# Kernel tuning notes

Measured on AMD Instinct MI355X. Metric: run time of the kernel, lower is better.

Reference implementation:

```python
import jax, jax.numpy as jnp
import numpy as np
from jax import lax


def setup_inputs() -> dict:
    key = jax.random.key(0)
    k1, k2 = jax.random.split(key)
    B, T, D = 32, 4096, 256
    x = jax.random.normal(k1, (B, T, D), dtype=jnp.float32)
    logit_alpha = jax.random.normal(k2, (D,), dtype=jnp.float32)
    return {"x": x, "logit_alpha": logit_alpha}


def _ema_scan(x, alpha):
    # Linear recurrence y_t = a_t * y_{t-1} + b_t is associative; use a
    # log-depth parallel scan over T instead of a sequential loop.
    B, T, D = x.shape
    one_minus_alpha = 1.0 - alpha  # [D]
    # y_0 = x_0  ->  a_0 = 0, b_0 = x_0 ; for t>=1: a_t = alpha, b_t = (1-alpha)*x_t
    a = jnp.concatenate(
        [jnp.zeros((B, 1, D), x.dtype), jnp.broadcast_to(alpha, (B, T - 1, D))],
        axis=1,
    )
    b = jnp.concatenate([x[:, :1, :], one_minus_alpha * x[:, 1:, :]], axis=1)

    def combine(e1, e2):
        a1, b1 = e1
        a2, b2 = e2
        return a1 * a2, a2 * b1 + b2

    _, y = lax.associative_scan(combine, (a, b), axis=1)
    return y


def reference(x, logit_alpha):
    # x: [B, T, D]; per-feature alpha in (0,1)
    alpha = jax.nn.sigmoid(logit_alpha)  # [D]
    return _ema_scan(x, alpha)
```

## Files before the change

kernel.cpp:

```cpp
#include <hip/hip_runtime.h>

#define B_  32
#define T_  4096
#define D_  256
#define D4_ 64

typedef float f32x4 __attribute__((ext_vector_type(4)));

__device__ __forceinline__ f32x4 sigmoid4(f32x4 v) {
    f32x4 r;
    r[0] = 1.0f / (1.0f + expf(-v[0]));
    r[1] = 1.0f / (1.0f + expf(-v[1]));
    r[2] = 1.0f / (1.0f + expf(-v[2]));
    r[3] = 1.0f / (1.0f + expf(-v[3]));
    return r;
}

__global__ __launch_bounds__(256) void ema_carry(
    const f32x4* __restrict__ x, const f32x4* __restrict__ la,
    f32x4* __restrict__ E, int NC, int L) {
    const int wid  = threadIdx.x >> 6;
    const int lane = threadIdx.x & 63;
    const int g = blockIdx.x * 4 + wid;
    const int b = g / NC;
    const int c = g % NC;

    const f32x4 al = sigmoid4(la[lane]);
    const f32x4 om = 1.0f - al;

    size_t idx = ((size_t)b * T_ + (size_t)c * L) * D4_ + lane;
    f32x4 y = 0.0f;
    int i0 = 0;
    if (c == 0) {
        y = x[idx];
        idx += D4_;
        i0 = 1;
    }
    #pragma unroll 8
    for (int i = i0; i < L; ++i) {
        y = al * y + om * x[idx];
        idx += D4_;
    }
    E[(size_t)g * D4_ + lane] = y;
}

__global__ __launch_bounds__(256) void ema_apply(
    const f32x4* __restrict__ x, const f32x4* __restrict__ la,
    const f32x4* __restrict__ E, f32x4* __restrict__ yout,
    int NC, int L, int log2L) {
    const int wid  = threadIdx.x >> 6;
    const int lane = threadIdx.x & 63;
    const int g = blockIdx.x * 4 + wid;
    const int b = g / NC;
    const int c = g % NC;

    const f32x4 al = sigmoid4(la[lane]);
    const f32x4 om = 1.0f - al;

    f32x4 aL = al;
    for (int k = 0; k < log2L; ++k) aL = aL * aL;
    const f32x4 aL2 = aL * aL;
    const f32x4 aL4 = aL2 * aL2;
    const f32x4 aL8 = aL4 * aL4;

    const f32x4* Eb = E + ((size_t)b * NC) * D4_ + lane;
    f32x4 H = 0.0f;
    int j = 0;
    for (; j + 8 <= c; j += 8) {
        f32x4 e0 = Eb[(size_t)(j + 0) * D4_];
        f32x4 e1 = Eb[(size_t)(j + 1) * D4_];
        f32x4 e2 = Eb[(size_t)(j + 2) * D4_];
        f32x4 e3 = Eb[(size_t)(j + 3) * D4_];
        f32x4 e4 = Eb[(size_t)(j + 4) * D4_];
        f32x4 e5 = Eb[(size_t)(j + 5) * D4_];
        f32x4 e6 = Eb[(size_t)(j + 6) * D4_];
        f32x4 e7 = Eb[(size_t)(j + 7) * D4_];
        f32x4 t = e0;
        t = t * aL + e1;
        t = t * aL + e2;
        t = t * aL + e3;
        t = t * aL + e4;
        t = t * aL + e5;
        t = t * aL + e6;
        t = t * aL + e7;
        H = aL8 * H + t;
    }
    for (; j < c; ++j)
        H = aL * H + Eb[(size_t)j * D4_];

    size_t idx = ((size_t)b * T_ + (size_t)c * L) * D4_ + lane;
    f32x4 acc = H;
    int i0 = 0;
    if (c == 0) {
        acc = x[idx];
        __builtin_nontemporal_store(acc, &yout[idx]);
        idx += D4_;
        i0 = 1;
    }
    #pragma unroll 8
    for (int i = i0; i < L; ++i) {
        acc = al * acc + om * x[idx];
        __builtin_nontemporal_store(acc, &yout[idx]);
        idx += D4_;
    }
}

extern "C" void kernel_launch(void* const* d_in, const int* in_sizes, int n_in,
                              void* d_out, int out_size, void* d_ws, size_t ws_size,
                              hipStream_t stream) {
    const f32x4* x  = (const f32x4*)d_in[0];
    const f32x4* la = (const f32x4*)d_in[1];
    f32x4* out = (f32x4*)d_out;

    int NC = 128;
    while (NC > 1 && (size_t)B_ * NC * D_ * sizeof(float) > ws_size) NC >>= 1;
    const int L = T_ / NC;
    int log2L = 0;
    while ((1 << log2L) < L) ++log2L;

    f32x4* E = (f32x4*)d_ws;
    const int ntasks = B_ * NC;
    dim3 blk(256);
    dim3 grd(ntasks / 4);

    ema_carry<<<grd, blk, 0, stream>>>(x, la, E, NC, L);
    ema_apply<<<grd, blk, 0, stream>>>(x, la, E, out, NC, L, log2L);
}
```

Measured before the change: 74.80 us.

## Restructure EMA as local scan plus carry fixup pass over output

Replaces the carry-then-recompute scheme with a first pass that writes the locally scanned output and chunk carries, and a second pass that adds the propagated carry times powers of alpha to the stored output. This removes the second read of x and the recurrence recompute in the apply pass, but adds a read-modify-write of the output. The chunk count is halved, which reduces carry work but also the number of parallel waves.

```diff
diff --git a/kernel.cpp b/kernel.cpp
--- a/kernel.cpp
+++ b/kernel.cpp
@@ -16,9 +16,9 @@
     return r;
 }
 
-__global__ __launch_bounds__(256) void ema_carry(
+__global__ __launch_bounds__(256) void ema_local(
     const f32x4* __restrict__ x, const f32x4* __restrict__ la,
-    f32x4* __restrict__ E, int NC, int L) {
+    f32x4* __restrict__ y, f32x4* __restrict__ E, int NC, int L) {
     const int wid  = threadIdx.x >> 6;
     const int lane = threadIdx.x & 63;
     const int g = blockIdx.x * 4 + wid;
@@ -29,33 +29,35 @@
     const f32x4 om = 1.0f - al;
 
     size_t idx = ((size_t)b * T_ + (size_t)c * L) * D4_ + lane;
-    f32x4 y = 0.0f;
+    f32x4 acc = 0.0f;
     int i0 = 0;
     if (c == 0) {
-        y = x[idx];
+        acc = __builtin_nontemporal_load(&x[idx]);
+        y[idx] = acc;
         idx += D4_;
         i0 = 1;
     }
     #pragma unroll 8
     for (int i = i0; i < L; ++i) {
-        y = al * y + om * x[idx];
+        f32x4 xv = __builtin_nontemporal_load(&x[idx]);
+        acc = al * acc + om * xv;
+        y[idx] = acc;
         idx += D4_;
     }
-    E[(size_t)g * D4_ + lane] = y;
+    E[(size_t)g * D4_ + lane] = acc;
 }
 
-__global__ __launch_bounds__(256) void ema_apply(
-    const f32x4* __restrict__ x, const f32x4* __restrict__ la,
-    const f32x4* __restrict__ E, f32x4* __restrict__ yout,
-    int NC, int L, int log2L) {
+__global__ __launch_bounds__(256) void ema_fixup(
+    const f32x4* __restrict__ la, const f32x4* __restrict__ E,
+    f32x4* __restrict__ y, int NC, int L, int log2L) {
     const int wid  = threadIdx.x >> 6;
     const int lane = threadIdx.x & 63;
     const int g = blockIdx.x * 4 + wid;
     const int b = g / NC;
     const int c = g % NC;
+    if (c == 0) return;
 
     const f32x4 al = sigmoid4(la[lane]);
-    const f32x4 om = 1.0f - al;
 
     f32x4 aL = al;
     for (int k = 0; k < log2L; ++k) aL = aL * aL;
@@ -89,18 +91,13 @@
         H = aL * H + Eb[(size_t)j * D4_];
 
     size_t idx = ((size_t)b * T_ + (size_t)c * L) * D4_ + lane;
-    f32x4 acc = H;
-    int i0 = 0;
-    if (c == 0) {
-        acc = x[idx];
-        __builtin_nontemporal_store(acc, &yout[idx]);
-        idx += D4_;
-        i0 = 1;
-    }
+    f32x4 coef = al;
     #pragma unroll 8
-    for (int i = i0; i < L; ++i) {
-        acc = al * acc + om * x[idx];
-        __builtin_nontemporal_store(acc, &yout[idx]);
+    for (int i = 0; i < L; ++i) {
+        f32x4 v = y[idx];
+        v = v + coef * H;
+        y[idx] = v;
+        coef = coef * al;
         idx += D4_;
     }
 }
@@ -112,7 +109,7 @@
     const f32x4* la = (const f32x4*)d_in[1];
     f32x4* out = (f32x4*)d_out;
 
-    int NC = 128;
+    int NC = 64;
     while (NC > 1 && (size_t)B_ * NC * D_ * sizeof(float) > ws_size) NC >>= 1;
     const int L = T_ / NC;
     int log2L = 0;
@@ -123,6 +120,6 @@
     dim3 blk(256);
     dim3 grd(ntasks / 4);
 
-    ema_carry<<<grd, blk, 0, stream>>>(x, la, E, NC, L);
-    ema_apply<<<grd, blk, 0, stream>>>(x, la, E, out, NC, L, log2L);
+    ema_local<<<grd, blk, 0, stream>>>(x, la, out, E, NC, L);
+    ema_fixup<<<grd, blk, 0, stream>>>(la, E, out, NC, L, log2L);
 }
```

Result: slower. 94.29 us (+26.0%).
